# Kernel optimization log

Hardware: AMD Instinct MI355X
Metric: run time of the kernel (lower is better)

Reference implementation:

```python
import jax, jax.numpy as jnp
import numpy as np

B, C, Q, D = 64, 512, 64, 256  # D = 2 * hidden_size; similarity weight has 3*D = 768 entries


def _length_mask(key, batch, seqlen):
    # realistic padding masks: each row has a random valid prefix length in [seqlen//2, seqlen]
    lens = jax.random.randint(key, (batch,), seqlen // 2, seqlen + 1)
    return (jnp.arange(seqlen)[None, :] < lens[:, None]).astype(jnp.int32)


def setup_inputs() -> dict:
    key = jax.random.key(0)
    k1, k2, k3, k4, k5 = jax.random.split(key, 5)
    context = jax.random.normal(k1, (B, C, D), dtype=jnp.float32)
    question = jax.random.normal(k2, (B, Q, D), dtype=jnp.float32)
    context_mask = _length_mask(k3, B, C)
    question_mask = _length_mask(k4, B, Q)
    w = jax.random.normal(k5, (3 * D,), dtype=jnp.float32) * (1.0 / np.sqrt(3 * D))
    return {"context": context, "question": question,
            "context_mask": context_mask, "question_mask": question_mask, "w": w}


def reference(context, question, context_mask, question_mask, w):
    d = context.shape[-1]
    # Linear([c, q, c*q]) with no bias decomposes exactly into three terms.
    w_c, w_q, w_m = w[:d], w[d:2 * d], w[2 * d:]
    sim = ((context @ w_c)[:, :, None]                      # [B, C, 1]
           + (question @ w_q)[:, None, :]                   # [B, 1, Q]
           + jnp.einsum('bcd,bqd->bcq', context * w_m, question))  # [B, C, Q]
    neg = jnp.finfo(sim.dtype).min
    # context-to-query attention (mask question positions)
    sim_q = jnp.where(question_mask[:, None, :] != 0, sim, neg)
    a = jax.nn.softmax(sim_q, axis=2)                        # [B, C, Q]
    c2q = jnp.einsum('bcq,bqd->bcd', a, question)            # [B, C, D]
    # query-to-context attention (max over Q, mask context positions)
    sim_max = jnp.max(sim, axis=2)                           # [B, C]
    sim_max = jnp.where(context_mask != 0, sim_max, neg)
    b = jax.nn.softmax(sim_max, axis=1)                      # [B, C]
    q2c = jnp.einsum('bc,bcd->bd', b, context)[:, None, :]   # [B, 1, D]
    q2c = jnp.broadcast_to(q2c, context.shape)               # [B, C, D]
    g = jnp.concatenate([context, c2q, context * c2q, context * q2c], axis=-1)
    return g
```

## Files before the change

### kernel.cpp

```cpp
#include <hip/hip_runtime.h>
#include <hip/hip_bf16.h>
#include <float.h>

#define B_ 64
#define C_ 512
#define Q_ 64
#define D_ 256

typedef _Float16 f16x8 __attribute__((ext_vector_type(8)));
typedef float f32x4 __attribute__((ext_vector_type(4)));

union U4H8 { uint4 u; f16x8 h; };
union UH2 { _Float16 h[2]; uint32_t u; };

__device__ __forceinline__ uint32_t packh2(float a, float b) {
  UH2 v; v.h[0] = (_Float16)a; v.h[1] = (_Float16)b; return v.u;
}

__device__ __forceinline__ float wred_sum(float v) {
#pragma unroll
  for (int off = 32; off > 0; off >>= 1) v += __shfl_xor(v, off, 64);
  return v;
}
__device__ __forceinline__ float wred_max(float v) {
#pragma unroll
  for (int off = 32; off > 0; off >>= 1) v = fmaxf(v, __shfl_xor(v, off, 64));
  return v;
}

__global__ __launch_bounds__(256) void k_rowdot(const float* __restrict__ src,
                                                const float* __restrict__ wgt,
                                                float* __restrict__ out, int nrows) {
  int wv = threadIdx.x >> 6, ln = threadIdx.x & 63;
  int row = blockIdx.x * 4 + wv;
  if (row >= nrows) return;
  float4 s4 = *(const float4*)(src + (size_t)row * D_ + 4 * ln);
  float4 w4 = *(const float4*)(wgt + 4 * ln);
  float p = s4.x * w4.x + s4.y * w4.y + s4.z * w4.z + s4.w * w4.w;
  p = wred_sum(p);
  if (ln == 0) out[row] = p;
}

__global__ __launch_bounds__(256) void k_prepack(const float* __restrict__ qst,
                                                 const float* __restrict__ w,
                                                 uint32_t* __restrict__ qraw_img,
                                                 uint32_t* __restrict__ qT_img,
                                                 float* __restrict__ qwq) {
  const int b = blockIdx.x;
  const int sub = blockIdx.y;
  const int t = threadIdx.x;
  const float* qb = qst + (size_t)b * Q_ * D_;
#pragma unroll
  for (int it = 0; it < 8; ++it) {
    int idx = sub * 2048 + it * 256 + t;
    int q = idx >> 7, jp = idx & 127;
    float2 v = *(const float2*)(qb + q * D_ + 2 * jp);
    int ch = jp >> 2;
    int phys = (ch & ~7) | ((ch & 7) ^ (q & 7));
    qraw_img[(size_t)b * 8192 + q * 128 + phys * 4 + (jp & 3)] = packh2(v.x, v.y);
  }
  {
    int d = sub * 64 + (t >> 2);
    uint32_t* dst = qT_img + (size_t)b * 8192 + d * 32;
#pragma unroll
    for (int k = 0; k < 2; ++k) {
      int qc = (t & 3) * 2 + k;
      uint32_t tmp[4];
#pragma unroll
      for (int e = 0; e < 4; ++e) {
        int q0 = qc * 8 + e * 2;
        tmp[e] = packh2(qb[q0 * D_ + d], qb[(q0 + 1) * D_ + d]);
      }
      int pc = qc ^ (d & 7);
      *(uint4*)(dst + pc * 4) = uint4{tmp[0], tmp[1], tmp[2], tmp[3]};
    }
  }
  if (sub == 0) {
    int q = t >> 2, sl = t & 3;
    float p = 0.f;
#pragma unroll
    for (int i = 0; i < 16; ++i) {
      float4 v = *(const float4*)(qb + q * D_ + sl * 64 + i * 4);
      float4 ww = *(const float4*)(w + D_ + sl * 64 + i * 4);
      p += v.x * ww.x + v.y * ww.y + v.z * ww.z + v.w * ww.w;
    }
    p += __shfl_xor(p, 1, 64);
    p += __shfl_xor(p, 2, 64);
    if (sl == 0) qwq[b * Q_ + q] = p;
  }
}

__global__ __launch_bounds__(256, 4) void k_sim(
    const float* __restrict__ ctx, const int* __restrict__ qmask,
    const int* __restrict__ cmask, const float* __restrict__ w,
    const float* __restrict__ qwq_g, const uint32_t* __restrict__ qraw_img,
    ushort* __restrict__ P_img, float* __restrict__ part,
    float* __restrict__ pmax_g, float* __restrict__ psum_g) {
  __shared__ __align__(16) ushort qraw[Q_ * D_];
  __shared__ float qwq_l[Q_];
  __shared__ int   qml_l[Q_];
  __shared__ __align__(16) float sred2[64];
  __shared__ float psum_w[4];
  __shared__ __align__(16) float pvLDS[4][256];

  const int bid = blockIdx.x;
  const int b = bid & 63;
  const int c0 = (bid >> 6) * 64;
  const int t = threadIdx.x;
  const int wv = t >> 6, ln = t & 63;
  const int lc = ln & 15;
  const int lg = ln >> 4;
  const int c0w = c0 + wv * 16;

  {
    const uint32_t* qr_src = qraw_img + (size_t)b * 8192;
#pragma unroll
    for (int i = 0; i < 8; ++i)
      __builtin_amdgcn_global_load_lds(
          (const __attribute__((address_space(1))) uint32_t*)(qr_src + i * 1024 + t * 4),
          (__attribute__((address_space(3))) uint32_t*)((uint32_t*)qraw + i * 1024 + t * 4),
          16, 0, 0);
  }

  f16x8 bfrag[8];
  float cwc_p = 0.f;
  const float* crow = ctx + ((size_t)b * C_ + c0w + lc) * D_;
#pragma unroll
  for (int kk = 0; kk < 8; ++kk) {
    int kb = kk * 32 + lg * 8;
    float4 cv0 = *(const float4*)(crow + kb);
    float4 cv1 = *(const float4*)(crow + kb + 4);
    float4 wc0 = *(const float4*)(w + kb);
    float4 wc1 = *(const float4*)(w + kb + 4);
    float4 wm0 = *(const float4*)(w + 2 * D_ + kb);
    float4 wm1 = *(const float4*)(w + 2 * D_ + kb + 4);
    cwc_p += cv0.x * wc0.x + cv0.y * wc0.y + cv0.z * wc0.z + cv0.w * wc0.w
           + cv1.x * wc1.x + cv1.y * wc1.y + cv1.z * wc1.z + cv1.w * wc1.w;
    bfrag[kk][0] = (_Float16)(cv0.x * wm0.x);
    bfrag[kk][1] = (_Float16)(cv0.y * wm0.y);
    bfrag[kk][2] = (_Float16)(cv0.z * wm0.z);
    bfrag[kk][3] = (_Float16)(cv0.w * wm0.w);
    bfrag[kk][4] = (_Float16)(cv1.x * wm1.x);
    bfrag[kk][5] = (_Float16)(cv1.y * wm1.y);
    bfrag[kk][6] = (_Float16)(cv1.z * wm1.z);
    bfrag[kk][7] = (_Float16)(cv1.w * wm1.w);
  }
  float cwc = cwc_p;
  cwc += __shfl_xor(cwc, 16, 64);
  cwc += __shfl_xor(cwc, 32, 64);

  if (t < Q_) { qwq_l[t] = qwq_g[b * Q_ + t]; qml_l[t] = qmask[b * Q_ + t]; }
  __syncthreads();

  f32x4 sacc[4];
#pragma unroll
  for (int tq = 0; tq < 4; ++tq) sacc[tq] = f32x4{0.f, 0.f, 0.f, 0.f};
#pragma unroll
  for (int tq = 0; tq < 4; ++tq) {
    int q = 16 * tq + lc;
#pragma unroll
    for (int kk = 0; kk < 8; ++kk) {
      int ch = lg + 4 * kk;
      int phys = (ch & ~7) | ((ch & 7) ^ (q & 7));
      U4H8 a; a.u = *(const uint4*)((const char*)qraw + q * 512 + phys * 16);
      sacc[tq] = __builtin_amdgcn_mfma_f32_16x16x32_f16(a.h, bfrag[kk], sacc[tq], 0, 0, 0);
    }
  }

  float vals[4][4];
  float rmax = -FLT_MAX;
#pragma unroll
  for (int tq = 0; tq < 4; ++tq) {
    float4 qw4 = *(const float4*)(qwq_l + 16 * tq + 4 * lg);
#pragma unroll
    for (int r = 0; r < 4; ++r) {
      float qv = (r == 0) ? qw4.x : (r == 1) ? qw4.y : (r == 2) ? qw4.z : qw4.w;
      vals[tq][r] = sacc[tq][r] + cwc + qv;
      rmax = fmaxf(rmax, vals[tq][r]);
    }
  }
  rmax = fmaxf(rmax, __shfl_xor(rmax, 16, 64));
  rmax = fmaxf(rmax, __shfl_xor(rmax, 32, 64));

  float mmax = -FLT_MAX;
#pragma unroll
  for (int tq = 0; tq < 4; ++tq) {
    int4 qm4 = *(const int4*)(qml_l + 16 * tq + 4 * lg);
#pragma unroll
    for (int r = 0; r < 4; ++r) {
      int m = (r == 0) ? qm4.x : (r == 1) ? qm4.y : (r == 2) ? qm4.z : qm4.w;
      vals[tq][r] = m ? vals[tq][r] : -FLT_MAX;
      mmax = fmaxf(mmax, vals[tq][r]);
    }
  }
  mmax = fmaxf(mmax, __shfl_xor(mmax, 16, 64));
  mmax = fmaxf(mmax, __shfl_xor(mmax, 32, 64));
  float esum = 0.f;
#pragma unroll
  for (int tq = 0; tq < 4; ++tq)
#pragma unroll
    for (int r = 0; r < 4; ++r) {
      vals[tq][r] = __expf(vals[tq][r] - mmax);
      esum += vals[tq][r];
    }
  esum += __shfl_xor(esum, 16, 64);
  esum += __shfl_xor(esum, 32, 64);
  float inv = 1.f / esum;
  char* pdst = (char*)(P_img + ((size_t)bid * 4 + wv) * 1024);
#pragma unroll
  for (int tq = 0; tq < 4; ++tq) {
    uint32_t p01 = packh2(vals[tq][0] * inv, vals[tq][1] * inv);
    uint32_t p23 = packh2(vals[tq][2] * inv, vals[tq][3] * inv);
    int qb4 = 16 * tq + 4 * lg;
    *(uint2*)(pdst + lc * 128 + qb4 * 2) = uint2{p01, p23};
  }

  if (ln < 16) {
    int cm = cmask[b * C_ + c0w + lc];
    sred2[wv * 16 + lc] = cm ? rmax : -FLT_MAX;
  }
  __syncthreads();
  float M_loc = -FLT_MAX;
#pragma unroll
  for (int i = 0; i < 16; ++i) {
    float4 v4 = *(const float4*)(sred2 + 4 * i);
    M_loc = fmaxf(M_loc, fmaxf(fmaxf(v4.x, v4.y), fmaxf(v4.z, v4.w)));
  }
  float4 pvec{0.f, 0.f, 0.f, 0.f};
  float ps = 0.f;
  const float* cbase = ctx + ((size_t)b * C_ + c0w) * D_ + 4 * ln;
#pragma unroll 4
  for (int r = 0; r < 16; ++r) {
    float e = __expf(sred2[wv * 16 + r] - M_loc);
    ps += e;
    float4 cv = *(const float4*)(cbase + r * D_);
    pvec.x += e * cv.x; pvec.y += e * cv.y;
    pvec.z += e * cv.z; pvec.w += e * cv.w;
  }
  *(float4*)(&pvLDS[wv][4 * ln]) = pvec;
  if (ln == 0) psum_w[wv] = ps;
  __syncthreads();
  {
    float s = pvLDS[0][t] + pvLDS[1][t] + pvLDS[2][t] + pvLDS[3][t];
    part[((size_t)b * 8 + (bid >> 6)) * D_ + t] = s;
  }
  if (t == 0) {
    pmax_g[b * 8 + (bid >> 6)] = M_loc;
    psum_g[b * 8 + (bid >> 6)] = psum_w[0] + psum_w[1] + psum_w[2] + psum_w[3];
  }
}

__global__ __launch_bounds__(256, 4) void k_c2q(
    const float* __restrict__ ctx, const uint32_t* __restrict__ qT_img,
    const ushort* __restrict__ P_img, const float* __restrict__ part,
    const float* __restrict__ pmax_g, const float* __restrict__ psum_g,
    float* __restrict__ g) {
  __shared__ __align__(16) ushort qT[D_ * Q_];
  __shared__ float q2c_l[D_];

  const int bid = blockIdx.x;
  const int b = bid & 63;
  const int c0 = (bid >> 6) * 64;
  const int t = threadIdx.x;
  const int wv = t >> 6, ln = t & 63;
  const int lc = ln & 15;
  const int lg = ln >> 4;
  const int c0w = c0 + wv * 16;

  {
    const uint32_t* qt_src = qT_img + (size_t)b * 8192;
#pragma unroll
    for (int i = 0; i < 8; ++i)
      __builtin_amdgcn_global_load_lds(
          (const __attribute__((address_space(1))) uint32_t*)(qt_src + i * 1024 + t * 4),
          (__attribute__((address_space(3))) uint32_t*)((uint32_t*)qT + i * 1024 + t * 4),
          16, 0, 0);
  }
  const char* psrc = (const char*)(P_img + ((size_t)bid * 4 + wv) * 1024);
  U4H8 pf0, pf1;
  pf0.u = *(const uint4*)(psrc + lc * 128 + lg * 16);
  pf1.u = *(const uint4*)(psrc + lc * 128 + lg * 16 + 64);
  {
    float M = -FLT_MAX;
#pragma unroll
    for (int k = 0; k < 8; ++k) M = fmaxf(M, pmax_g[b * 8 + k]);
    float den = 0.f, num = 0.f;
#pragma unroll
    for (int k = 0; k < 8; ++k) {
      float sc = __expf(pmax_g[b * 8 + k] - M);
      den += psum_g[b * 8 + k] * sc;
      num += part[((size_t)b * 8 + k) * D_ + t] * sc;
    }
    q2c_l[t] = num / den;
  }
  __syncthreads();

  const float* crow2 = ctx + ((size_t)b * C_ + c0w + lc) * D_;
  float* grow = g + ((size_t)b * C_ + c0w + lc) * (4 * D_);
#pragma unroll 4
  for (int dt = 0; dt < 16; ++dt) {
    f32x4 acc = f32x4{0.f, 0.f, 0.f, 0.f};
    {
      int d = dt * 16 + lc;
      int phys0 = lg ^ (d & 7);
      int phys1 = (lg + 4) ^ (d & 7);
      U4H8 aq0; aq0.u = *(const uint4*)((const char*)qT + d * 128 + phys0 * 16);
      U4H8 aq1; aq1.u = *(const uint4*)((const char*)qT + d * 128 + phys1 * 16);
      acc = __builtin_amdgcn_mfma_f32_16x16x32_f16(aq0.h, pf0.h, acc, 0, 0, 0);
      acc = __builtin_amdgcn_mfma_f32_16x16x32_f16(aq1.h, pf1.h, acc, 0, 0, 0);
    }
    int dcol = dt * 16 + 4 * lg;
    float4 cvv = *(const float4*)(crow2 + dcol);
    float4 q4 = *(const float4*)(q2c_l + dcol);
    *(float4*)(grow + dcol) = cvv;
    float4 c2qv{acc[0], acc[1], acc[2], acc[3]};
    *(float4*)(grow + D_ + dcol) = c2qv;
    float4 p2{cvv.x * c2qv.x, cvv.y * c2qv.y, cvv.z * c2qv.z, cvv.w * c2qv.w};
    *(float4*)(grow + 2 * D_ + dcol) = p2;
    float4 p3{cvv.x * q4.x, cvv.y * q4.y, cvv.z * q4.z, cvv.w * q4.w};
    *(float4*)(grow + 3 * D_ + dcol) = p3;
  }
}

__global__ __launch_bounds__(256) void k_q2c_bs(const float* __restrict__ ctx,
                                                const float* __restrict__ simmax,
                                                const int* __restrict__ cmask,
                                                float* __restrict__ part) {
  int b = blockIdx.x, ch = blockIdx.y, t = threadIdx.x;
  int wv = t >> 6, ln = t & 63;
  __shared__ float bls[C_];
  __shared__ float sred[4];
  __shared__ float ssum[4];
  float v0 = simmax[b * C_ + t], v1 = simmax[b * C_ + 256 + t];
  if (!cmask[b * C_ + t]) v0 = -FLT_MAX;
  if (!cmask[b * C_ + 256 + t]) v1 = -FLT_MAX;
  float mx = wred_max(fmaxf(v0, v1));
  if (ln == 0) sred[wv] = mx;
  __syncthreads();
  float bm = fmaxf(fmaxf(sred[0], sred[1]), fmaxf(sred[2], sred[3]));
  float e0 = __expf(v0 - bm), e1 = __expf(v1 - bm);
  float ps = wred_sum(e0 + e1);
  if (ln == 0) ssum[wv] = ps;
  __syncthreads();
  float bs = ssum[0] + ssum[1] + ssum[2] + ssum[3];
  float invbs = 1.f / bs;
  bls[t] = e0 * invbs;
  bls[256 + t] = e1 * invbs;
  __syncthreads();
  float acc = 0.f;
  int cbeg = ch * 64;
#pragma unroll 4
  for (int c = cbeg; c < cbeg + 64; ++c)
    acc += bls[c] * ctx[((size_t)b * C_ + c) * D_ + t];
  part[((size_t)b * 8 + ch) * D_ + t] = acc;
}

__global__ __launch_bounds__(256, 2) void k_main_fb(
    const float* __restrict__ ctx, const float* __restrict__ qst,
    const int* __restrict__ qmask, const float* __restrict__ w,
    const float* __restrict__ qwq_g, float* __restrict__ g,
    float* __restrict__ simmax_g) {
  __shared__ __align__(16) ushort qraw[Q_ * D_];
  __shared__ __align__(16) ushort qT[D_ * Q_];
  __shared__ __align__(16) ushort pbuf[4][16 * Q_];
  __shared__ float qwq_l[Q_];
  __shared__ int   qml_l[Q_];

  const int bid = blockIdx.x;
  const int b = bid & 63;
  const int c0 = (bid >> 6) * 64;
  const int t = threadIdx.x;
  const int wv = t >> 6, ln = t & 63;
  const int lc = ln & 15;
  const int lg = ln >> 4;
  const int c0w = c0 + wv * 16;
  const float* qb = qst + (size_t)b * Q_ * D_;

  f16x8 bfrag[8];
  float cwc_p = 0.f;
  const float* crow = ctx + ((size_t)b * C_ + c0w + lc) * D_;
  float* grow0 = g + ((size_t)b * C_ + c0w + lc) * (4 * D_);
#pragma unroll
  for (int kk = 0; kk < 8; ++kk) {
    int kb = kk * 32 + lg * 8;
    float4 cv0 = *(const float4*)(crow + kb);
    float4 cv1 = *(const float4*)(crow + kb + 4);
    float4 wc0 = *(const float4*)(w + kb);
    float4 wc1 = *(const float4*)(w + kb + 4);
    float4 wm0 = *(const float4*)(w + 2 * D_ + kb);
    float4 wm1 = *(const float4*)(w + 2 * D_ + kb + 4);
    cwc_p += cv0.x * wc0.x + cv0.y * wc0.y + cv0.z * wc0.z + cv0.w * wc0.w
           + cv1.x * wc1.x + cv1.y * wc1.y + cv1.z * wc1.z + cv1.w * wc1.w;
    bfrag[kk][0] = (_Float16)(cv0.x * wm0.x);
    bfrag[kk][1] = (_Float16)(cv0.y * wm0.y);
    bfrag[kk][2] = (_Float16)(cv0.z * wm0.z);
    bfrag[kk][3] = (_Float16)(cv0.w * wm0.w);
    bfrag[kk][4] = (_Float16)(cv1.x * wm1.x);
    bfrag[kk][5] = (_Float16)(cv1.y * wm1.y);
    bfrag[kk][6] = (_Float16)(cv1.z * wm1.z);
    bfrag[kk][7] = (_Float16)(cv1.w * wm1.w);
    *(float4*)(grow0 + kb) = cv0;
    *(float4*)(grow0 + kb + 4) = cv1;
  }
  float cwc = cwc_p;
  cwc += __shfl_xor(cwc, 16, 64);
  cwc += __shfl_xor(cwc, 32, 64);

#pragma unroll 4
  for (int it = 0; it < 32; ++it) {
    int idx = it * 256 + t;
    int q = idx >> 7, jp = idx & 127;
    float2 v = *(const float2*)(qb + q * D_ + 2 * jp);
    int ch = jp >> 2;
    int phys = (ch & ~7) | ((ch & 7) ^ (q & 7));
    *(uint32_t*)((char*)qraw + q * 512 + phys * 16 + (jp & 3) * 4) = packh2(v.x, v.y);
  }
#pragma unroll 4
  for (int it = 0; it < 32; ++it) {
    int q = t & 63;
    int jp = (t >> 6) + 4 * it;
    float2 v = *(const float2*)(qb + q * D_ + 2 * jp);
    int d0 = 2 * jp, d1 = d0 + 1;
    UH2 h0; h0.h[0] = (_Float16)v.x;
    UH2 h1; h1.h[0] = (_Float16)v.y;
    *(ushort*)((char*)qT + d0 * 128 + (((q >> 3) ^ (d0 & 7)) << 4) + (q & 7) * 2) = (ushort)(h0.u & 0xffff);
    *(ushort*)((char*)qT + d1 * 128 + (((q >> 3) ^ (d1 & 7)) << 4) + (q & 7) * 2) = (ushort)(h1.u & 0xffff);
  }
  if (t < Q_) { qwq_l[t] = qwq_g[b * Q_ + t]; qml_l[t] = qmask[b * Q_ + t]; }
  __syncthreads();

  f32x4 sacc[4];
#pragma unroll
  for (int tq = 0; tq < 4; ++tq) sacc[tq] = f32x4{0.f, 0.f, 0.f, 0.f};
#pragma unroll
  for (int tq = 0; tq < 4; ++tq) {
    int q = 16 * tq + lc;
#pragma unroll
    for (int kk = 0; kk < 8; ++kk) {
      int ch = lg + 4 * kk;
      int phys = (ch & ~7) | ((ch & 7) ^ (q & 7));
      U4H8 a; a.u = *(const uint4*)((const char*)qraw + q * 512 + phys * 16);
      sacc[tq] = __builtin_amdgcn_mfma_f32_16x16x32_f16(a.h, bfrag[kk], sacc[tq], 0, 0, 0);
    }
  }
  float vals[4][4];
  float rmax = -FLT_MAX;
#pragma unroll
  for (int tq = 0; tq < 4; ++tq) {
    float4 qw4 = *(const float4*)(qwq_l + 16 * tq + 4 * lg);
#pragma unroll
    for (int r = 0; r < 4; ++r) {
      float qv = (r == 0) ? qw4.x : (r == 1) ? qw4.y : (r == 2) ? qw4.z : qw4.w;
      vals[tq][r] = sacc[tq][r] + cwc + qv;
      rmax = fmaxf(rmax, vals[tq][r]);
    }
  }
  rmax = fmaxf(rmax, __shfl_xor(rmax, 16, 64));
  rmax = fmaxf(rmax, __shfl_xor(rmax, 32, 64));
  if (ln < 16) simmax_g[b * C_ + c0w + lc] = rmax;
  float mmax = -FLT_MAX;
#pragma unroll
  for (int tq = 0; tq < 4; ++tq) {
    int4 qm4 = *(const int4*)(qml_l + 16 * tq + 4 * lg);
#pragma unroll
    for (int r = 0; r < 4; ++r) {
      int m = (r == 0) ? qm4.x : (r == 1) ? qm4.y : (r == 2) ? qm4.z : qm4.w;
      vals[tq][r] = m ? vals[tq][r] : -FLT_MAX;
      mmax = fmaxf(mmax, vals[tq][r]);
    }
  }
  mmax = fmaxf(mmax, __shfl_xor(mmax, 16, 64));
  mmax = fmaxf(mmax, __shfl_xor(mmax, 32, 64));
  float esum = 0.f;
#pragma unroll
  for (int tq = 0; tq < 4; ++tq)
#pragma unroll
    for (int r = 0; r < 4; ++r) {
      vals[tq][r] = __expf(vals[tq][r] - mmax);
      esum += vals[tq][r];
    }
  esum += __shfl_xor(esum, 16, 64);
  esum += __shfl_xor(esum, 32, 64);
  float inv = 1.f / esum;
#pragma unroll
  for (int tq = 0; tq < 4; ++tq) {
    uint32_t p01 = packh2(vals[tq][0] * inv, vals[tq][1] * inv);
    uint32_t p23 = packh2(vals[tq][2] * inv, vals[tq][3] * inv);
    int qb4 = 16 * tq + 4 * lg;
    int phys = ((qb4 >> 3) ^ (lc & 7));
    char* dst = (char*)pbuf[wv] + lc * 128 + phys * 16 + (qb4 & 7) * 2;
    *(uint2*)dst = uint2{p01, p23};
  }
  f16x8 pfragB[2];
#pragma unroll
  for (int ks = 0; ks < 2; ++ks) {
    int phys = (lg + 4 * ks) ^ (lc & 7);
    U4H8 a; a.u = *(const uint4*)((const char*)pbuf[wv] + lc * 128 + phys * 16);
    pfragB[ks] = a.h;
  }
  const float* crow2 = ctx + ((size_t)b * C_ + c0w + lc) * D_;
  float* grow = g + ((size_t)b * C_ + c0w + lc) * (4 * D_);
#pragma unroll 4
  for (int dt = 0; dt < 16; ++dt) {
    f32x4 acc = f32x4{0.f, 0.f, 0.f, 0.f};
#pragma unroll
    for (int ks = 0; ks < 2; ++ks) {
      int d = dt * 16 + lc;
      int phys = (lg + 4 * ks) ^ (d & 7);
      U4H8 aq; aq.u = *(const uint4*)((const char*)qT + d * 128 + phys * 16);
      acc = __builtin_amdgcn_mfma_f32_16x16x32_f16(aq.h, pfragB[ks], acc, 0, 0, 0);
    }
    int dcol = dt * 16 + 4 * lg;
    float4 cvv = *(const float4*)(crow2 + dcol);
    float4 c2qv{acc[0], acc[1], acc[2], acc[3]};
    *(float4*)(grow + D_ + dcol) = c2qv;
    float4 p2{cvv.x * c2qv.x, cvv.y * c2qv.y, cvv.z * c2qv.z, cvv.w * c2qv.w};
    *(float4*)(grow + 2 * D_ + dcol) = p2;
  }
}

__global__ __launch_bounds__(256) void k_g3q(const float* __restrict__ ctx,
                                             const float* __restrict__ part,
                                             float* __restrict__ g) {
  int b = blockIdx.x, ch = blockIdx.y, t = threadIdx.x;
  __shared__ float q2c_l[D_];
  float s = 0.f;
#pragma unroll
  for (int k = 0; k < 8; ++k) s += part[((size_t)b * 8 + k) * D_ + t];
  q2c_l[t] = s;
  __syncthreads();
  int d4 = t & 63;
  int ro = t >> 6;
  float4 qv = *(const float4*)(q2c_l + 4 * d4);
#pragma unroll 4
  for (int it = 0; it < 16; ++it) {
    int c = ch * 64 + it * 4 + ro;
    float4 cv = *(const float4*)(ctx + ((size_t)b * C_ + c) * D_ + 4 * d4);
    float4 o{cv.x * qv.x, cv.y * qv.y, cv.z * qv.z, cv.w * qv.w};
    *(float4*)(g + ((size_t)b * C_ + c) * (4 * D_) + 3 * D_ + 4 * d4) = o;
  }
}

extern "C" void kernel_launch(void* const* d_in, const int* in_sizes, int n_in,
                              void* d_out, int out_size, void* d_ws, size_t ws_size,
                              hipStream_t stream) {
  const float* ctx   = (const float*)d_in[0];
  const float* qst   = (const float*)d_in[1];
  const int*   cmask = (const int*)d_in[2];
  const int*   qmask = (const int*)d_in[3];
  const float* w     = (const float*)d_in[4];
  float* g  = (float*)d_out;
  float* ws = (float*)d_ws;

  float*    qwq      = ws;
  float*    simmax   = ws + 4096;
  float*    part     = ws + 36864;
  float*    pmax_g   = ws + 167936;
  float*    psum_g   = ws + 168448;
  uint32_t* qraw_img = (uint32_t*)(ws + 168960);
  uint32_t* qT_img   = (uint32_t*)(ws + 693248);
  ushort*   P_img    = (ushort*)(ws + 1217536);
  const size_t need_bytes = (size_t)(1217536 + 1048576) * 4;

  if (ws_size >= need_bytes) {
    k_prepack<<<dim3(B_, 4), 256, 0, stream>>>(qst, w, qraw_img, qT_img, qwq);
    k_sim<<<dim3(512), 256, 0, stream>>>(ctx, qmask, cmask, w, qwq, qraw_img,
                                         P_img, part, pmax_g, psum_g);
    k_c2q<<<dim3(512), 256, 0, stream>>>(ctx, qT_img, P_img, part,
                                         pmax_g, psum_g, g);
  } else {
    k_rowdot<<<dim3(B_ * Q_ / 4), 256, 0, stream>>>(qst, w + D_, qwq, B_ * Q_);
    k_main_fb<<<dim3(512), 256, 0, stream>>>(ctx, qst, qmask, w, qwq, g, simmax);
    k_q2c_bs<<<dim3(B_, 8), 256, 0, stream>>>(ctx, simmax, cmask, part);
    k_g3q<<<dim3(B_, 8), 256, 0, stream>>>(ctx, part, g);
  }
}
```

Before: 57.65 us.

## Move context copy into sim kernel and split c2q over D halves

```diff
diff --git a/kernel.cpp b/kernel.cpp
--- a/kernel.cpp
+++ b/kernel.cpp
@@ -95,7 +95,8 @@
     const int* __restrict__ cmask, const float* __restrict__ w,
     const float* __restrict__ qwq_g, const uint32_t* __restrict__ qraw_img,
     ushort* __restrict__ P_img, float* __restrict__ part,
-    float* __restrict__ pmax_g, float* __restrict__ psum_g) {
+    float* __restrict__ pmax_g, float* __restrict__ psum_g,
+    float* __restrict__ g) {
   __shared__ __align__(16) ushort qraw[Q_ * D_];
   __shared__ float qwq_l[Q_];
   __shared__ int   qml_l[Q_];
@@ -229,11 +230,13 @@
   float4 pvec{0.f, 0.f, 0.f, 0.f};
   float ps = 0.f;
   const float* cbase = ctx + ((size_t)b * C_ + c0w) * D_ + 4 * ln;
+  float* g0base = g + ((size_t)b * C_ + c0w) * (4 * D_) + 4 * ln;
 #pragma unroll 4
   for (int r = 0; r < 16; ++r) {
     float e = __expf(sred2[wv * 16 + r] - M_loc);
     ps += e;
     float4 cv = *(const float4*)(cbase + r * D_);
+    *(float4*)(g0base + r * (4 * D_)) = cv;
     pvec.x += e * cv.x; pvec.y += e * cv.y;
     pvec.z += e * cv.z; pvec.w += e * cv.w;
   }
@@ -255,12 +258,14 @@
     const ushort* __restrict__ P_img, const float* __restrict__ part,
     const float* __restrict__ pmax_g, const float* __restrict__ psum_g,
     float* __restrict__ g) {
-  __shared__ __align__(16) ushort qT[D_ * Q_];
+  __shared__ __align__(16) ushort qT[128 * Q_];
   __shared__ float q2c_l[D_];
 
-  const int bid = blockIdx.x;
-  const int b = bid & 63;
-  const int c0 = (bid >> 6) * 64;
+  const int bid2 = blockIdx.x;
+  const int b = bid2 & 63;
+  const int tile = (bid2 >> 6) & 7;
+  const int h = bid2 >> 9;
+  const int c0 = tile * 64;
   const int t = threadIdx.x;
   const int wv = t >> 6, ln = t & 63;
   const int lc = ln & 15;
@@ -268,15 +273,15 @@
   const int c0w = c0 + wv * 16;
 
   {
-    const uint32_t* qt_src = qT_img + (size_t)b * 8192;
-#pragma unroll
-    for (int i = 0; i < 8; ++i)
+    const uint32_t* qt_src = qT_img + (size_t)b * 8192 + h * 4096;
+#pragma unroll
+    for (int i = 0; i < 4; ++i)
       __builtin_amdgcn_global_load_lds(
           (const __attribute__((address_space(1))) uint32_t*)(qt_src + i * 1024 + t * 4),
           (__attribute__((address_space(3))) uint32_t*)((uint32_t*)qT + i * 1024 + t * 4),
           16, 0, 0);
   }
-  const char* psrc = (const char*)(P_img + ((size_t)bid * 4 + wv) * 1024);
+  const char* psrc = (const char*)(P_img + ((size_t)(tile * 64 + b) * 4 + wv) * 1024);
   U4H8 pf0, pf1;
   pf0.u = *(const uint4*)(psrc + lc * 128 + lg * 16);
   pf1.u = *(const uint4*)(psrc + lc * 128 + lg * 16 + 64);
@@ -298,21 +303,22 @@
   const float* crow2 = ctx + ((size_t)b * C_ + c0w + lc) * D_;
   float* grow = g + ((size_t)b * C_ + c0w + lc) * (4 * D_);
 #pragma unroll 4
-  for (int dt = 0; dt < 16; ++dt) {
+  for (int j = 0; j < 8; ++j) {
+    int dt = h * 8 + j;
     f32x4 acc = f32x4{0.f, 0.f, 0.f, 0.f};
     {
       int d = dt * 16 + lc;
+      int dl = d - h * 128;
       int phys0 = lg ^ (d & 7);
       int phys1 = (lg + 4) ^ (d & 7);
-      U4H8 aq0; aq0.u = *(const uint4*)((const char*)qT + d * 128 + phys0 * 16);
-      U4H8 aq1; aq1.u = *(const uint4*)((const char*)qT + d * 128 + phys1 * 16);
+      U4H8 aq0; aq0.u = *(const uint4*)((const char*)qT + dl * 128 + phys0 * 16);
+      U4H8 aq1; aq1.u = *(const uint4*)((const char*)qT + dl * 128 + phys1 * 16);
       acc = __builtin_amdgcn_mfma_f32_16x16x32_f16(aq0.h, pf0.h, acc, 0, 0, 0);
       acc = __builtin_amdgcn_mfma_f32_16x16x32_f16(aq1.h, pf1.h, acc, 0, 0, 0);
     }
     int dcol = dt * 16 + 4 * lg;
     float4 cvv = *(const float4*)(crow2 + dcol);
     float4 q4 = *(const float4*)(q2c_l + dcol);
-    *(float4*)(grow + dcol) = cvv;
     float4 c2qv{acc[0], acc[1], acc[2], acc[3]};
     *(float4*)(grow + D_ + dcol) = c2qv;
     float4 p2{cvv.x * c2qv.x, cvv.y * c2qv.y, cvv.z * c2qv.z, cvv.w * c2qv.w};
@@ -565,9 +571,9 @@
   if (ws_size >= need_bytes) {
     k_prepack<<<dim3(B_, 4), 256, 0, stream>>>(qst, w, qraw_img, qT_img, qwq);
     k_sim<<<dim3(512), 256, 0, stream>>>(ctx, qmask, cmask, w, qwq, qraw_img,
-                                         P_img, part, pmax_g, psum_g);
-    k_c2q<<<dim3(512), 256, 0, stream>>>(ctx, qT_img, P_img, part,
-                                         pmax_g, psum_g, g);
+                                         P_img, part, pmax_g, psum_g, g);
+    k_c2q<<<dim3(1024), 256, 0, stream>>>(ctx, qT_img, P_img, part,
+                                          pmax_g, psum_g, g);
   } else {
     k_rowdot<<<dim3(B_ * Q_ / 4), 256, 0, stream>>>(qst, w + D_, qwq, B_ * Q_);
     k_main_fb<<<dim3(512), 256, 0, stream>>>(ctx, qst, qmask, w, qwq, g, simmax);
```

New measurement: 60.17 us. 1.04x slower.
